# Kernel optimization log

Hardware: AMD Instinct MI355X
Metric: run time of the kernel (lower is better)

## Reference

```python
import jax, jax.numpy as jnp
import numpy as np

HEADS = 8
NQ = 4  # n_qubits


def _apply_rx(state, q, theta):
    # state: (M,2,2,2,2) complex, theta: (M,)
    c = jnp.cos(theta / 2).astype(jnp.complex64)
    s = (-1j * jnp.sin(theta / 2)).astype(jnp.complex64)
    g = jnp.stack([jnp.stack([c, s], -1), jnp.stack([s, c], -1)], -2)  # (M,2,2)
    st = jnp.moveaxis(state, 1 + q, 1)
    st = jnp.einsum('mab,mb...->ma...', g, st)
    return jnp.moveaxis(st, 1, 1 + q)


def _apply_cnot(state, c, t):
    st = jnp.moveaxis(state, [1 + c, 1 + t], [1, 2])  # (M,2(ctrl),2(tgt),...)
    st = jnp.concatenate([st[:, :1], st[:, 1:, ::-1]], axis=1)
    return jnp.moveaxis(st, [1, 2], [1 + c, 1 + t])


def vqc(x, weights):
    # x: (M,4) embedding angles; weights: (L,4) layer RX angles
    M = x.shape[0]
    state = jnp.zeros((M, 2, 2, 2, 2), jnp.complex64).at[:, 0, 0, 0, 0].set(1.0)
    for q in range(NQ):  # AngleEmbedding (RX)
        state = _apply_rx(state, q, x[:, q])
    for l in range(weights.shape[0]):  # BasicEntanglerLayers
        for q in range(NQ):
            state = _apply_rx(state, q, jnp.broadcast_to(weights[l, q], (M,)))
        for q in range(NQ):
            state = _apply_cnot(state, q, (q + 1) % NQ)
    probs = state.real ** 2 + state.imag ** 2  # (M,2,2,2,2)
    z = [jnp.moveaxis(probs, 1 + q, 1)[:, 0].sum((1, 2, 3))
         - jnp.moveaxis(probs, 1 + q, 1)[:, 1].sum((1, 2, 3)) for q in range(NQ)]
    return jnp.stack(z, -1)  # (M,4) PauliZ expvals


def setup_inputs() -> dict:
    key = jax.random.key(0)
    ks = jax.random.split(key, 24)
    B, S, E = 16, 512, 512
    D = E // HEADS
    f = jax.random.normal
    inp = {
        'query': f(ks[0], (B, S, E), jnp.float32),
        'key': f(ks[1], (B, S, E), jnp.float32),
        'value': f(ks[2], (B, S, E), jnp.float32),
        'mask': jnp.ones((B, S, S), jnp.int32),
        'Wq_in': f(ks[3], (NQ, D), jnp.float32) / np.sqrt(D),
        'bq_in': f(ks[4], (NQ,), jnp.float32) / np.sqrt(D),
        'Wk_in': f(ks[5], (NQ, D), jnp.float32) / np.sqrt(D),
        'bk_in': f(ks[6], (NQ,), jnp.float32) / np.sqrt(D),
        'Wv_in': f(ks[7], (NQ, D), jnp.float32) / np.sqrt(D),
        'bv_in': f(ks[8], (NQ,), jnp.float32) / np.sqrt(D),
        'wvq': f(ks[9], (1, NQ), jnp.float32),
        'wvk': f(ks[10], (1, NQ), jnp.float32),
        'wvv': f(ks[11], (1, NQ), jnp.float32),
        'Wq': f(ks[12], (D, NQ), jnp.float32) / np.sqrt(NQ),
        'bq': f(ks[13], (D,), jnp.float32) / np.sqrt(NQ),
        'Wk': f(ks[14], (D, NQ), jnp.float32) / np.sqrt(NQ),
        'bk': f(ks[15], (D,), jnp.float32) / np.sqrt(NQ),
        'Wv': f(ks[16], (D, NQ), jnp.float32) / np.sqrt(NQ),
        'bv': f(ks[17], (D,), jnp.float32) / np.sqrt(NQ),
        'Wo': f(ks[18], (E, 2 * E), jnp.float32) / np.sqrt(2 * E),
        'bo': f(ks[19], (E,), jnp.float32) / np.sqrt(2 * E),
    }
    return inp


def reference(query, key, value, mask, Wq_in, bq_in, Wk_in, bk_in, Wv_in, bv_in,
              wvq, wvk, wvv, Wq, bq, Wk, bk, Wv, bv, Wo, bo):
    B, S, E = query.shape
    H = HEADS
    D = E // H

    def project(x, W_in, b_in, w_vqc, W_out, b_out):
        xh = x.reshape(B, S, H, D)
        xin = jnp.einsum('bshd,qd->bshq', xh, W_in) + b_in  # (B,S,H,NQ)
        xq = vqc(xin.reshape(-1, NQ), w_vqc).reshape(B, S, H, NQ)
        return jnp.einsum('bshq,dq->bshd', xq, W_out) + b_out  # (B,S,H,D)

    Q = project(query, Wq_in, bq_in, wvq, Wq, bq)
    K = project(key, Wk_in, bk_in, wvk, Wk, bk)
    V = project(value, Wv_in, bv_in, wvv, Wv, bv)

    energy = jnp.einsum('bqhd,bkhd->bhqk', Q, K)
    # NOTE: original masked_fill result is discarded (no-op); scale is depth/2
    # due to Python precedence (depth**1/2 == depth/2). Reproduced faithfully.
    attn = jax.nn.softmax(energy / (D / 2.0), axis=-1)
    out = jnp.einsum('bhqv,bvhd->bqhd', attn, V).reshape(B, S, H * D)
    Qf = Q.reshape(B, S, H * D)
    cat = jnp.concatenate([Qf, out], axis=-1)  # (B,S,2E)
    return cat @ Wo.T + bo
```

## Files before the change

### kernel.cpp

```cpp
#include <hip/hip_runtime.h>
#include <hip/hip_bf16.h>

#define B_ 16
#define S_ 512
#define E_ 512
#define H_ 8
#define D_ 64

typedef __hip_bfloat16 bf16;
typedef unsigned short u16;
typedef __attribute__((ext_vector_type(8))) short short8;
typedef __attribute__((ext_vector_type(4))) float floatx4;

__device__ __forceinline__ u16 f2b(float x) {
    bf16 h = __float2bfloat16(x);
    return *reinterpret_cast<u16*>(&h);
}
__device__ __forceinline__ short8 ld8(const u16* p) { return *(const short8*)p; }

#define PROJ_BLOCKS 49152

__global__ __launch_bounds__(256) void proj_kernel(
    const float* __restrict__ q_in, const float* __restrict__ k_in, const float* __restrict__ v_in,
    const float* __restrict__ Wq_in, const float* __restrict__ bq_in,
    const float* __restrict__ Wk_in, const float* __restrict__ bk_in,
    const float* __restrict__ Wv_in, const float* __restrict__ bv_in,
    const float* __restrict__ wvq, const float* __restrict__ wvk, const float* __restrict__ wvv,
    const float* __restrict__ Wq, const float* __restrict__ bq,
    const float* __restrict__ Wk, const float* __restrict__ bk,
    const float* __restrict__ Wv, const float* __restrict__ bv,
    const float* __restrict__ Wo, u16* __restrict__ Wb,
    u16* __restrict__ Qb, u16* __restrict__ Kb, u16* __restrict__ Vb)
{
    if (blockIdx.x >= PROJ_BLOCKS) {
        const int i = ((blockIdx.x - PROJ_BLOCKS) * 256 + threadIdx.x) * 8;
        const float4 a = *(const float4*)&Wo[i];
        const float4 b4 = *(const float4*)&Wo[i + 4];
        u16 tmp[8] __attribute__((aligned(16)));
        tmp[0] = f2b(a.x); tmp[1] = f2b(a.y); tmp[2] = f2b(a.z); tmp[3] = f2b(a.w);
        tmp[4] = f2b(b4.x); tmp[5] = f2b(b4.y); tmp[6] = f2b(b4.z); tmp[7] = f2b(b4.w);
        *(short8*)&Wb[i] = *(short8*)tmp;
        return;
    }

    const int wave = threadIdx.x >> 6;
    const int lane = threadIdx.x & 63;
    const int g = blockIdx.x * 4 + wave;
    const int p = g >> 16;
    const int m = g & 0xFFFF;
    const int h = m & 7;
    const int s = (m >> 3) & 511;
    const int b = m >> 12;

    const float *X, *Win, *bin, *wv, *Wout, *bout;
    u16* dst;
    if (p == 0)      { X = q_in; Win = Wq_in; bin = bq_in; wv = wvq; Wout = Wq; bout = bq; dst = Qb; }
    else if (p == 1) { X = k_in; Win = Wk_in; bin = bk_in; wv = wvk; Wout = Wk; bout = bk; dst = Kb; }
    else             { X = v_in; Win = Wv_in; bin = bv_in; wv = wvv; Wout = Wv; bout = bv; dst = Vb; }

    const int q = lane >> 4;
    const int dsub = lane & 15;

    const float4 x4 = *(const float4*)(X + ((size_t)(b * S_ + s)) * E_ + h * 64 + dsub * 4);
    const float4 w4 = *(const float4*)(Win + q * 64 + dsub * 4);

    float part = x4.x * w4.x + x4.y * w4.y + x4.z * w4.z + x4.w * w4.w;
#pragma unroll
    for (int off = 8; off >= 1; off >>= 1)
        part += __shfl_xor(part, off, 64);

    const float theta = part + bin[q] + wv[q];
    const float c = __cosf(theta);

    const float c0 = __shfl(c, 0, 64);
    const float c1 = __shfl(c, 16, 64);
    const float c2 = __shfl(c, 32, 64);
    const float c3 = __shfl(c, 48, 64);

    const float tt = c2 * c3;
    const float z1 = c0 * c1;
    const float z0 = c1 * tt;
    const float z2 = z1 * c2;
    const float z3 = z1 * tt;

    const float4 wo = *(const float4*)&Wout[lane * 4];
    const float out = fmaf(z0, wo.x, fmaf(z1, wo.y, fmaf(z2, wo.z, fmaf(z3, wo.w, bout[lane]))));
    dst[(((size_t)(b * H_ + h)) * S_ + s) * D_ + lane] = f2b(out);
}

__global__ __launch_bounds__(256) void attn_kernel(
    const u16* __restrict__ Qb, const u16* __restrict__ Kb, const u16* __restrict__ Vb,
    u16* __restrict__ Ob)
{
    __shared__ __align__(16) u16 Ks[64][72];
    __shared__ __align__(16) u16 Vt[64][72];
    __shared__ __align__(16) u16 Ps[4][16][72];

    const int t = threadIdx.x, lane = t & 63, w = t >> 6;
    const int bh = blockIdx.x >> 3;
    const int q0 = (blockIdx.x & 7) * 64;
    const int b = bh >> 3, h = bh & 7;

    const u16* Qp = Qb + (size_t)bh * (S_ * D_) + (size_t)q0 * D_;
    const u16* Kp = Kb + (size_t)bh * (S_ * D_);
    const u16* Vp = Vb + (size_t)bh * (S_ * D_);

    const int nl = lane & 15;
    const int kg = (lane >> 4) * 8;

    const short8 qa0 = ld8(&Qp[(w * 16 + nl) * 64 + kg]);
    const short8 qa1 = ld8(&Qp[(w * 16 + nl) * 64 + kg + 32]);

    floatx4 of[4];
    float l_run[4] = {0.f, 0.f, 0.f, 0.f};
#pragma unroll
    for (int nt = 0; nt < 4; ++nt) of[nt] = 0.f;

    const int vr0 = (t & 31) * 2, vc = (t >> 5) * 8;

    for (int ch = 0; ch < 8; ++ch) {
        __syncthreads();
        for (int i = t; i < 512; i += 256) {
            const int r = i & 63, c = (i >> 6) * 8;
            *(short8*)&Ks[r][c] = ld8(&Kp[(ch * 64 + r) * 64 + c]);
        }
        {
            short8 va = ld8(&Vp[(ch * 64 + vr0) * 64 + vc]);
            short8 vb = ld8(&Vp[(ch * 64 + vr0 + 1) * 64 + vc]);
#pragma unroll
            for (int j = 0; j < 8; ++j) {
                const unsigned pack = (u16)((short*)&va)[j] |
                                      ((unsigned)(u16)((short*)&vb)[j] << 16);
                *(unsigned*)&Vt[vc + j][vr0] = pack;
            }
        }
        __syncthreads();

        floatx4 sf[4];
#pragma unroll
        for (int nt = 0; nt < 4; ++nt) sf[nt] = 0.f;
#pragma unroll
        for (int nt = 0; nt < 4; ++nt) {
            sf[nt] = __builtin_amdgcn_mfma_f32_16x16x32_bf16(qa0, ld8(&Ks[nt * 16 + nl][kg]), sf[nt], 0, 0, 0);
            sf[nt] = __builtin_amdgcn_mfma_f32_16x16x32_bf16(qa1, ld8(&Ks[nt * 16 + nl][kg + 32]), sf[nt], 0, 0, 0);
        }

        const int prow = (lane >> 4) * 4;
#pragma unroll
        for (int nt = 0; nt < 4; ++nt) {
#pragma unroll
            for (int r = 0; r < 4; ++r) {
                const float pv = __expf(sf[nt][r] * 0.03125f);
                l_run[r] += pv;
                Ps[w][prow + r][nt * 16 + nl] = f2b(pv);
            }
        }

        const short8 pa0 = ld8(&Ps[w][nl][kg]);
        const short8 pa1 = ld8(&Ps[w][nl][kg + 32]);
#pragma unroll
        for (int nt = 0; nt < 4; ++nt) {
            of[nt] = __builtin_amdgcn_mfma_f32_16x16x32_bf16(pa0, ld8(&Vt[nt * 16 + nl][kg]), of[nt], 0, 0, 0);
            of[nt] = __builtin_amdgcn_mfma_f32_16x16x32_bf16(pa1, ld8(&Vt[nt * 16 + nl][kg + 32]), of[nt], 0, 0, 0);
        }
    }

    float inv[4];
#pragma unroll
    for (int r = 0; r < 4; ++r) {
        float sum = l_run[r];
#pragma unroll
        for (int off = 1; off < 16; off <<= 1) sum += __shfl_xor(sum, off, 64);
        inv[r] = 1.0f / sum;
    }
    const int srow = q0 + w * 16 + (lane >> 4) * 4;
#pragma unroll
    for (int r = 0; r < 4; ++r) {
        const size_t base = ((size_t)(b * S_ + srow + r)) * E_ + h * 64 + nl;
#pragma unroll
        for (int nt = 0; nt < 4; ++nt)
            Ob[base + nt * 16] = f2b(of[nt][r] * inv[r]);
    }
}

__global__ __launch_bounds__(256) void out_kernel(
    const u16* __restrict__ Qb, const u16* __restrict__ Ob,
    const u16* __restrict__ Wb, const float* __restrict__ bo,
    float* __restrict__ out)
{
    __shared__ __align__(16) u16 As[64][72];
    __shared__ __align__(16) u16 Bs[128][72];

    const int t = threadIdx.x, lane = t & 63, w = t >> 6;
    const int e0 = (blockIdx.x & 3) * 128;
    const int n0 = (blockIdx.x >> 2) * 64;
    const int wr = (w >> 1) * 32, wc = (w & 1) * 64;
    const int nl = lane & 15, kg = (lane >> 4) * 8;

    floatx4 acc[2][4];
#pragma unroll
    for (int i = 0; i < 2; ++i)
#pragma unroll
        for (int j = 0; j < 4; ++j) acc[i][j] = 0.f;

    for (int j0 = 0; j0 < 1024; j0 += 64) {
        for (int i = t; i < 512; i += 256) {
            const int r = i & 63, c = (i >> 6) * 8;
            const int n = n0 + r;
            const u16* src = (j0 < 512)
                ? &Qb[(((size_t)(n >> 9) * 8 + (j0 >> 6)) * 512 + (n & 511)) * 64 + c]
                : &Ob[(size_t)n * 512 + (j0 - 512) + c];
            *(short8*)&As[r][c] = ld8(src);
        }
        for (int i = t; i < 1024; i += 256) {
            const int r = i & 127, c = (i >> 7) * 8;
            *(short8*)&Bs[r][c] = ld8(&Wb[(size_t)(e0 + r) * 1024 + j0 + c]);
        }
        __syncthreads();

        short8 af[2][2], bfr[4][2];
#pragma unroll
        for (int mt = 0; mt < 2; ++mt) {
            af[mt][0] = ld8(&As[wr + mt * 16 + nl][kg]);
            af[mt][1] = ld8(&As[wr + mt * 16 + nl][kg + 32]);
        }
#pragma unroll
        for (int nt = 0; nt < 4; ++nt) {
            bfr[nt][0] = ld8(&Bs[wc + nt * 16 + nl][kg]);
            bfr[nt][1] = ld8(&Bs[wc + nt * 16 + nl][kg + 32]);
        }
#pragma unroll
        for (int mt = 0; mt < 2; ++mt)
#pragma unroll
            for (int nt = 0; nt < 4; ++nt) {
                acc[mt][nt] = __builtin_amdgcn_mfma_f32_16x16x32_bf16(af[mt][0], bfr[nt][0], acc[mt][nt], 0, 0, 0);
                acc[mt][nt] = __builtin_amdgcn_mfma_f32_16x16x32_bf16(af[mt][1], bfr[nt][1], acc[mt][nt], 0, 0, 0);
            }
        __syncthreads();
    }

    const int prow = (lane >> 4) * 4;
#pragma unroll
    for (int mt = 0; mt < 2; ++mt)
#pragma unroll
        for (int r = 0; r < 4; ++r) {
            const int n = n0 + wr + mt * 16 + prow + r;
#pragma unroll
            for (int nt = 0; nt < 4; ++nt) {
                const int e = e0 + wc + nt * 16 + nl;
                out[(size_t)n * 512 + e] = acc[mt][nt][r] + bo[e];
            }
        }
}

extern "C" void kernel_launch(void* const* d_in, const int* in_sizes, int n_in,
                              void* d_out, int out_size, void* d_ws, size_t ws_size,
                              hipStream_t stream)
{
    const float* q_in  = (const float*)d_in[0];
    const float* k_in  = (const float*)d_in[1];
    const float* v_in  = (const float*)d_in[2];
    const float* Wq_in = (const float*)d_in[4];
    const float* bq_in = (const float*)d_in[5];
    const float* Wk_in = (const float*)d_in[6];
    const float* bk_in = (const float*)d_in[7];
    const float* Wv_in = (const float*)d_in[8];
    const float* bv_in = (const float*)d_in[9];
    const float* wvq   = (const float*)d_in[10];
    const float* wvk   = (const float*)d_in[11];
    const float* wvv   = (const float*)d_in[12];
    const float* Wq    = (const float*)d_in[13];
    const float* bq    = (const float*)d_in[14];
    const float* Wk    = (const float*)d_in[15];
    const float* bk    = (const float*)d_in[16];
    const float* Wv    = (const float*)d_in[17];
    const float* bv    = (const float*)d_in[18];
    const float* Wo    = (const float*)d_in[19];
    const float* bo    = (const float*)d_in[20];

    u16* ws = (u16*)d_ws;
    u16* Qb = ws;
    u16* Kb = ws + (size_t)(1 << 22);
    u16* Vb = ws + (size_t)(2 << 22);
    u16* Ob = ws + (size_t)3 * (1 << 22);
    u16* Wb = ws + (size_t)4 * (1 << 22);

    proj_kernel<<<PROJ_BLOCKS + 256, 256, 0, stream>>>(q_in, k_in, v_in,
        Wq_in, bq_in, Wk_in, bk_in, Wv_in, bv_in,
        wvq, wvk, wvv, Wq, bq, Wk, bk, Wv, bv,
        Wo, Wb, Qb, Kb, Vb);
    attn_kernel<<<1024, 256, 0, stream>>>(Qb, Kb, Vb, Ob);
    out_kernel<<<512, 256, 0, stream>>>(Qb, Ob, Wb, bo, (float*)d_out);
}
```

Measured before the change: 225.9 us.

## Restructure projection to 4 threads per row and register-prefetch tiles in attention/GEMM

```diff
diff --git a/kernel.cpp b/kernel.cpp
--- a/kernel.cpp
+++ b/kernel.cpp
@@ -18,7 +18,13 @@
 }
 __device__ __forceinline__ short8 ld8(const u16* p) { return *(const short8*)p; }
 
-#define PROJ_BLOCKS 49152
+template<int CTRL>
+__device__ __forceinline__ float qperm(float x) {
+    return __builtin_bit_cast(float,
+        __builtin_amdgcn_update_dpp(0, __builtin_bit_cast(int, x), CTRL, 0xF, 0xF, true));
+}
+
+#define PROJ_ROW_BLOCKS 3072
 
 __global__ __launch_bounds__(256) void proj_kernel(
     const float* __restrict__ q_in, const float* __restrict__ k_in, const float* __restrict__ v_in,
@@ -32,8 +38,8 @@
     const float* __restrict__ Wo, u16* __restrict__ Wb,
     u16* __restrict__ Qb, u16* __restrict__ Kb, u16* __restrict__ Vb)
 {
-    if (blockIdx.x >= PROJ_BLOCKS) {
-        const int i = ((blockIdx.x - PROJ_BLOCKS) * 256 + threadIdx.x) * 8;
+    if (blockIdx.x >= PROJ_ROW_BLOCKS) {
+        const int i = ((blockIdx.x - PROJ_ROW_BLOCKS) * 256 + threadIdx.x) * 8;
         const float4 a = *(const float4*)&Wo[i];
         const float4 b4 = *(const float4*)&Wo[i + 4];
         u16 tmp[8] __attribute__((aligned(16)));
@@ -43,14 +49,13 @@
         return;
     }
 
-    const int wave = threadIdx.x >> 6;
-    const int lane = threadIdx.x & 63;
-    const int g = blockIdx.x * 4 + wave;
-    const int p = g >> 16;
-    const int m = g & 0xFFFF;
-    const int h = m & 7;
-    const int s = (m >> 3) & 511;
-    const int b = m >> 12;
+    __shared__ __align__(16) float sWin[256];
+    __shared__ __align__(16) float sWout[256];
+    __shared__ __align__(16) float sbout[64];
+    __shared__ float4 sbw;
+
+    const int t = threadIdx.x;
+    const int p = blockIdx.x >> 10;
 
     const float *X, *Win, *bin, *wv, *Wout, *bout;
     u16* dst;
@@ -58,34 +63,62 @@
     else if (p == 1) { X = k_in; Win = Wk_in; bin = bk_in; wv = wvk; Wout = Wk; bout = bk; dst = Kb; }
     else             { X = v_in; Win = Wv_in; bin = bv_in; wv = wvv; Wout = Wv; bout = bv; dst = Vb; }
 
-    const int q = lane >> 4;
-    const int dsub = lane & 15;
-
-    const float4 x4 = *(const float4*)(X + ((size_t)(b * S_ + s)) * E_ + h * 64 + dsub * 4);
-    const float4 w4 = *(const float4*)(Win + q * 64 + dsub * 4);
-
-    float part = x4.x * w4.x + x4.y * w4.y + x4.z * w4.z + x4.w * w4.w;
-#pragma unroll
-    for (int off = 8; off >= 1; off >>= 1)
-        part += __shfl_xor(part, off, 64);
-
-    const float theta = part + bin[q] + wv[q];
-    const float c = __cosf(theta);
-
-    const float c0 = __shfl(c, 0, 64);
-    const float c1 = __shfl(c, 16, 64);
-    const float c2 = __shfl(c, 32, 64);
-    const float c3 = __shfl(c, 48, 64);
-
+    sWin[t] = Win[t];
+    sWout[t] = Wout[t];
+    if (t < 64) sbout[t] = bout[t];
+    if (t == 0) sbw = make_float4(bin[0] + wv[0], bin[1] + wv[1],
+                                  bin[2] + wv[2], bin[3] + wv[3]);
+    __syncthreads();
+
+    const int j = t & 3;
+    const int m = (blockIdx.x & 1023) * 64 + (t >> 2);
+    const int d0 = j * 16;
+
+    const float* xp = X + (size_t)m * 64 + d0;
+    float4 xv[4];
+#pragma unroll
+    for (int i = 0; i < 4; ++i) xv[i] = *(const float4*)(xp + i * 4);
+
+    float part[4] = {0.f, 0.f, 0.f, 0.f};
+#pragma unroll
+    for (int i = 0; i < 4; ++i) {
+#pragma unroll
+        for (int q = 0; q < 4; ++q) {
+            const float4 w4 = *(const float4*)&sWin[q * 64 + d0 + i * 4];
+            part[q] = fmaf(xv[i].x, w4.x, fmaf(xv[i].y, w4.y,
+                      fmaf(xv[i].z, w4.z, fmaf(xv[i].w, w4.w, part[q]))));
+        }
+    }
+#pragma unroll
+    for (int q = 0; q < 4; ++q) {
+        part[q] += qperm<0xB1>(part[q]);
+        part[q] += qperm<0x4E>(part[q]);
+    }
+
+    const float4 bw = sbw;
+    const float c0 = __cosf(part[0] + bw.x);
+    const float c1 = __cosf(part[1] + bw.y);
+    const float c2 = __cosf(part[2] + bw.z);
+    const float c3 = __cosf(part[3] + bw.w);
     const float tt = c2 * c3;
     const float z1 = c0 * c1;
     const float z0 = c1 * tt;
     const float z2 = z1 * c2;
     const float z3 = z1 * tt;
 
-    const float4 wo = *(const float4*)&Wout[lane * 4];
-    const float out = fmaf(z0, wo.x, fmaf(z1, wo.y, fmaf(z2, wo.z, fmaf(z3, wo.w, bout[lane]))));
-    dst[(((size_t)(b * H_ + h)) * S_ + s) * D_ + lane] = f2b(out);
+    const int b = m >> 12, s = (m >> 3) & 511, h = m & 7;
+    u16* op = dst + ((size_t)(b * 4096 + h * 512 + s)) * 64 + d0;
+
+    u16 tmp[16] __attribute__((aligned(16)));
+#pragma unroll
+    for (int d = 0; d < 16; ++d) {
+        const float4 wo = *(const float4*)&sWout[(d0 + d) * 4];
+        const float o = fmaf(z0, wo.x, fmaf(z1, wo.y,
+                        fmaf(z2, wo.z, fmaf(z3, wo.w, sbout[d0 + d]))));
+        tmp[d] = f2b(o);
+    }
+    *(short8*)op = *(short8*)tmp;
+    *(short8*)(op + 8) = *(short8*)(tmp + 8);
 }
 
 __global__ __launch_bounds__(256) void attn_kernel(
@@ -116,23 +149,30 @@
 #pragma unroll
     for (int nt = 0; nt < 4; ++nt) of[nt] = 0.f;
 
+    const int rK = t & 63, cK = (t >> 6) * 8;
     const int vr0 = (t & 31) * 2, vc = (t >> 5) * 8;
+
+    short8 kA = ld8(&Kp[rK * 64 + cK]);
+    short8 kB = ld8(&Kp[rK * 64 + cK + 32]);
+    short8 vA = ld8(&Vp[vr0 * 64 + vc]);
+    short8 vB = ld8(&Vp[(vr0 + 1) * 64 + vc]);
 
     for (int ch = 0; ch < 8; ++ch) {
         __syncthreads();
-        for (int i = t; i < 512; i += 256) {
-            const int r = i & 63, c = (i >> 6) * 8;
-            *(short8*)&Ks[r][c] = ld8(&Kp[(ch * 64 + r) * 64 + c]);
-        }
-        {
-            short8 va = ld8(&Vp[(ch * 64 + vr0) * 64 + vc]);
-            short8 vb = ld8(&Vp[(ch * 64 + vr0 + 1) * 64 + vc]);
-#pragma unroll
-            for (int j = 0; j < 8; ++j) {
-                const unsigned pack = (u16)((short*)&va)[j] |
-                                      ((unsigned)(u16)((short*)&vb)[j] << 16);
-                *(unsigned*)&Vt[vc + j][vr0] = pack;
-            }
+        *(short8*)&Ks[rK][cK] = kA;
+        *(short8*)&Ks[rK][cK + 32] = kB;
+#pragma unroll
+        for (int jj = 0; jj < 8; ++jj) {
+            const unsigned pack = (u16)((short*)&vA)[jj] |
+                                  ((unsigned)(u16)((short*)&vB)[jj] << 16);
+            *(unsigned*)&Vt[vc + jj][vr0] = pack;
+        }
+        if (ch < 7) {
+            const int nb = (ch + 1) * 64;
+            kA = ld8(&Kp[(nb + rK) * 64 + cK]);
+            kB = ld8(&Kp[(nb + rK) * 64 + cK + 32]);
+            vA = ld8(&Vp[(nb + vr0) * 64 + vc]);
+            vB = ld8(&Vp[(nb + vr0 + 1) * 64 + vc]);
         }
         __syncthreads();
 
@@ -197,24 +237,46 @@
     const int wr = (w >> 1) * 32, wc = (w & 1) * 64;
     const int nl = lane & 15, kg = (lane >> 4) * 8;
 
+    const int rA = t & 63, cA = (t >> 6) * 8;
+    const int rB = t & 127, cB0 = (t >> 7) * 8;
+    const u16* wrow = &Wb[(size_t)(e0 + rB) * 1024];
+
     floatx4 acc[2][4];
 #pragma unroll
     for (int i = 0; i < 2; ++i)
 #pragma unroll
-        for (int j = 0; j < 4; ++j) acc[i][j] = 0.f;
+        for (int jq = 0; jq < 4; ++jq) acc[i][jq] = 0.f;
+
+    auto a_src = [&](int j0, int r, int c) -> const u16* {
+        const int n = n0 + r;
+        return (j0 < 512)
+            ? &Qb[(((size_t)(n >> 9) * 8 + (j0 >> 6)) * 512 + (n & 511)) * 64 + c]
+            : &Ob[(size_t)n * 512 + (j0 - 512) + c];
+    };
+
+    short8 aA = ld8(a_src(0, rA, cA));
+    short8 aB = ld8(a_src(0, rA, cA + 32));
+    short8 b0 = ld8(wrow + cB0);
+    short8 b1 = ld8(wrow + cB0 + 16);
+    short8 b2 = ld8(wrow + cB0 + 32);
+    short8 b3 = ld8(wrow + cB0 + 48);
 
     for (int j0 = 0; j0 < 1024; j0 += 64) {
-        for (int i = t; i < 512; i += 256) {
-            const int r = i & 63, c = (i >> 6) * 8;
-            const int n = n0 + r;
-            const u16* src = (j0 < 512)
-                ? &Qb[(((size_t)(n >> 9) * 8 + (j0 >> 6)) * 512 + (n & 511)) * 64 + c]
-                : &Ob[(size_t)n * 512 + (j0 - 512) + c];
-            *(short8*)&As[r][c] = ld8(src);
-        }
-        for (int i = t; i < 1024; i += 256) {
-            const int r = i & 127, c = (i >> 7) * 8;
-            *(short8*)&Bs[r][c] = ld8(&Wb[(size_t)(e0 + r) * 1024 + j0 + c]);
+        __syncthreads();
+        *(short8*)&As[rA][cA] = aA;
+        *(short8*)&As[rA][cA + 32] = aB;
+        *(short8*)&Bs[rB][cB0] = b0;
+        *(short8*)&Bs[rB][cB0 + 16] = b1;
+        *(short8*)&Bs[rB][cB0 + 32] = b2;
+        *(short8*)&Bs[rB][cB0 + 48] = b3;
+        if (j0 < 960) {
+            const int jn = j0 + 64;
+            aA = ld8(a_src(jn, rA, cA));
+            aB = ld8(a_src(jn, rA, cA + 32));
+            b0 = ld8(wrow + jn + cB0);
+            b1 = ld8(wrow + jn + cB0 + 16);
+            b2 = ld8(wrow + jn + cB0 + 32);
+            b3 = ld8(wrow + jn + cB0 + 48);
         }
         __syncthreads();
 
@@ -236,7 +298,6 @@
                 acc[mt][nt] = __builtin_amdgcn_mfma_f32_16x16x32_bf16(af[mt][0], bfr[nt][0], acc[mt][nt], 0, 0, 0);
                 acc[mt][nt] = __builtin_amdgcn_mfma_f32_16x16x32_bf16(af[mt][1], bfr[nt][1], acc[mt][nt], 0, 0, 0);
             }
-        __syncthreads();
     }
 
     const int prow = (lane >> 4) * 4;
@@ -285,7 +346,7 @@
     u16* Ob = ws + (size_t)3 * (1 << 22);
     u16* Wb = ws + (size_t)4 * (1 << 22);
 
-    proj_kernel<<<PROJ_BLOCKS + 256, 256, 0, stream>>>(q_in, k_in, v_in,
+    proj_kernel<<<PROJ_ROW_BLOCKS + 256, 256, 0, stream>>>(q_in, k_in, v_in,
         Wq_in, bq_in, Wk_in, bk_in, Wv_in, bv_in,
         wvq, wvk, wvv, Wq, bq, Wk, bk, Wv, bv,
         Wo, Wb, Qb, Kb, Vb);
```

Result: faster. 190.3 us (-15.8%).
